# Performance work log

Measured on AMD Instinct MI355X. Metric: run time of the kernel, lower is better.

Reference implementation:

```python
import jax, jax.numpy as jnp
import numpy as np
import math

B, N, D_MODEL, H, D_HEAD = 2, 2048, 1024, 16, 64
EPS = 1e-6

def setup_inputs() -> dict:
    key = jax.random.key(0)
    ks = jax.random.split(key, 6)
    s = 1.0 / math.sqrt(D_MODEL)
    return {
        "X": jax.random.normal(ks[0], (B, N, D_MODEL), dtype=jnp.float32),
        "Wq": jax.random.normal(ks[1], (D_MODEL, H * D_HEAD), dtype=jnp.float32) * s,
        "Wk": jax.random.normal(ks[2], (D_MODEL, H * D_HEAD), dtype=jnp.float32) * s,
        "Wv": jax.random.normal(ks[3], (D_MODEL, H * D_HEAD), dtype=jnp.float32) * s,
        "Wo": jax.random.normal(ks[4], (H * D_HEAD, D_MODEL), dtype=jnp.float32) * s,
        "bo": jnp.zeros((D_MODEL,), dtype=jnp.float32),
    }

def reference(X, Wq, Wk, Wv, Wo, bo):
    b, n, _ = X.shape
    # project and split heads -> [b, h, n, d_head]
    def heads(Y):
        return Y.reshape(b, n, H, D_HEAD).transpose(0, 2, 1, 3)
    Q = heads(X @ Wq)
    K = heads(X @ Wk)
    V = heads(X @ Wv)
    # per-head L2 normalization of Q and K
    Q = Q / (jnp.linalg.norm(Q, axis=-1, keepdims=True) + EPS)
    K = K / (jnp.linalg.norm(K, axis=-1, keepdims=True) + EPS)
    # scores [b, h, n, n]
    A = jnp.einsum("bhqd,bhkd->bhqk", Q, K) / math.sqrt(D_HEAD)
    causal = jnp.triu(jnp.ones((n, n), dtype=bool), k=1)
    A = jnp.where(causal, -jnp.inf, A)
    A = jax.nn.softmax(A, axis=-1)
    V_hat = jnp.einsum("bhqk,bhkd->bhqd", A, V)
    V_hat = V_hat.transpose(0, 2, 1, 3).reshape(b, n, H * D_HEAD)
    return V_hat @ Wo + bo
```

## Files before the change

kernel.cpp:

```cpp
#include <hip/hip_runtime.h>
#include <hip/hip_bf16.h>
#include <math.h>

#define BATCH 2
#define NSEQ  2048
#define DM    1024
#define NH    16
#define DH    64
#define EPS_N 1e-6f

typedef unsigned short u16;
typedef __attribute__((ext_vector_type(8))) short short8;
typedef __attribute__((ext_vector_type(8))) unsigned short u16x8;
typedef __attribute__((ext_vector_type(4))) unsigned short u16x4;
typedef __attribute__((ext_vector_type(4))) float f32x4;

__device__ __forceinline__ u16 f2bf(float x) {
  __hip_bfloat16 h = __float2bfloat16(x);
  return *reinterpret_cast<u16*>(&h);
}

__device__ __forceinline__ void gl_lds16(const u16* g, u16* lds_base) {
  __builtin_amdgcn_global_load_lds(
      (__attribute__((address_space(1))) void*)g,
      (__attribute__((address_space(3))) void*)lds_base, 16, 0, 0);
}

__global__ __launch_bounds__(256) void prep(
    const float* __restrict__ X,
    const float* __restrict__ w0, const float* __restrict__ w1,
    const float* __restrict__ w2, const float* __restrict__ w3,
    u16* __restrict__ Xb, u16* __restrict__ WT) {
  const int id = blockIdx.x, tid = threadIdx.x;
  if (id >= 1024) {
    size_t base = ((size_t)(id - 1024) * 256 + tid) * 8;
    float4 f0 = *(const float4*)&X[base];
    float4 f1 = *(const float4*)&X[base + 4];
    u16x8 v;
    v[0] = f2bf(f0.x); v[1] = f2bf(f0.y); v[2] = f2bf(f0.z); v[3] = f2bf(f0.w);
    v[4] = f2bf(f1.x); v[5] = f2bf(f1.y); v[6] = f2bf(f1.z); v[7] = f2bf(f1.w);
    *(u16x8*)&Xb[base] = v;
    return;
  }
  const int z = id >> 8, xy = id & 255, bx = xy & 15, by = xy >> 4;
  const float* in = (z == 0) ? w0 : (z == 1) ? w1 : (z == 2) ? w2 : w3;
  u16* o = WT + (size_t)z * DM * DM;
  __shared__ u16 T[64][65];
  const int n0 = bx * 64, k0 = by * 64;
  #pragma unroll
  for (int i = 0; i < 4; i++) {
    int c = tid + 256 * i, row = c >> 4, col4 = c & 15;
    float4 f = *(const float4*)&in[(size_t)(k0 + row) * DM + n0 + col4 * 4];
    T[row][col4 * 4 + 0] = f2bf(f.x);
    T[row][col4 * 4 + 1] = f2bf(f.y);
    T[row][col4 * 4 + 2] = f2bf(f.z);
    T[row][col4 * 4 + 3] = f2bf(f.w);
  }
  __syncthreads();
  #pragma unroll
  for (int i = 0; i < 2; i++) {
    int c = tid + 256 * i, row = c >> 3, col8 = c & 7;
    u16x8 v;
    #pragma unroll
    for (int e = 0; e < 8; e++) v[e] = T[col8 * 8 + e][row];
    *(u16x8*)&o[(size_t)(n0 + row) * DM + k0 + col8 * 8] = v;
  }
}

#define GEMM128_MAINLOOP(Aptr, Btptr)                                          \
  __shared__ u16 As[128 * 64];                                                 \
  __shared__ u16 Bs[128 * 64];                                                 \
  const int tid = threadIdx.x, w = tid >> 6, lane = tid & 63;                  \
  const int ml = lane & 15, quad = lane >> 4;                                  \
  const int m0 = blockIdx.y * 128, n0 = blockIdx.x * 128;                      \
  const int wm = w & 1, wn = w >> 1;                                           \
  const int srow = lane >> 3;                      \
  const int scol = ((lane & 7) ^ srow) * 8;         \
  f32x4 acc[4][4];                                                             \
  _Pragma("unroll") for (int mi = 0; mi < 4; mi++)                             \
    _Pragma("unroll") for (int ni = 0; ni < 4; ni++)                           \
      _Pragma("unroll") for (int e = 0; e < 4; e++) acc[mi][ni][e] = 0.f;      \
  for (int k0 = 0; k0 < DM; k0 += 64) {                                        \
    __syncthreads();                                                           \
    _Pragma("unroll") for (int L = 0; L < 4; L++) {                            \
      int I = w * 4 + L;                                                       \
      gl_lds16(Aptr  + (size_t)(m0 + I * 8 + srow) * DM + k0 + scol,           \
               As + I * 512);                                                  \
      gl_lds16(Btptr + (size_t)(n0 + I * 8 + srow) * DM + k0 + scol,           \
               Bs + I * 512);                                                  \
    }                                                                          \
    __syncthreads();                                                           \
    _Pragma("unroll") for (int kk = 0; kk < 64; kk += 32) {                    \
      const int kc = kk >> 3;                          \
      short8 am[4], bn[4];                                                     \
      _Pragma("unroll") for (int i = 0; i < 4; i++) {                          \
        int ra = wm * 64 + i * 16 + ml;                                        \
        int rb = wn * 64 + i * 16 + ml;                                        \
        am[i] = *(const short8*)&As[ra * 64 + (((quad + kc) ^ (ra & 7)) * 8)]; \
        bn[i] = *(const short8*)&Bs[rb * 64 + (((quad + kc) ^ (rb & 7)) * 8)]; \
      }                                                                        \
      _Pragma("unroll") for (int mi = 0; mi < 4; mi++)                         \
        _Pragma("unroll") for (int ni = 0; ni < 4; ni++)                       \
          acc[mi][ni] = __builtin_amdgcn_mfma_f32_16x16x32_bf16(               \
              am[mi], bn[ni], acc[mi][ni], 0, 0, 0);                           \
    }                                                                          \
  }

__global__ __launch_bounds__(256) void gemm_qkv128(
    const u16* __restrict__ Xb, const u16* __restrict__ WT,
    u16* __restrict__ Qo, u16* __restrict__ Ko, u16* __restrict__ Vt) {
  const u16* Bt = WT + (size_t)blockIdx.z * DM * DM;
  GEMM128_MAINLOOP(Xb, Bt)
  const int z = blockIdx.z;
  if (z < 2) {
    u16* OutQK = (z == 0) ? Qo : Ko;
    const float qsc = (z == 0) ? 0.125f : 1.0f;
    const int h = (n0 >> 6) + wn;
    #pragma unroll
    for (int mi = 0; mi < 4; mi++) {
      int mrow0 = m0 + wm * 64 + mi * 16 + quad * 4;
      int b = mrow0 >> 11, tok0 = mrow0 & (NSEQ - 1);
      #pragma unroll
      for (int r = 0; r < 4; r++) {
        float ss = 0.f;
        #pragma unroll
        for (int ni = 0; ni < 4; ni++) ss += acc[mi][ni][r] * acc[mi][ni][r];
        ss += __shfl_xor(ss, 1, 64);
        ss += __shfl_xor(ss, 2, 64);
        ss += __shfl_xor(ss, 4, 64);
        ss += __shfl_xor(ss, 8, 64);
        float sc = qsc / (sqrtf(ss) + EPS_N);
        #pragma unroll
        for (int ni = 0; ni < 4; ni++)
          OutQK[((size_t)(b * NH + h) * NSEQ + tok0 + r) * DH + ni * 16 + ml] =
              f2bf(acc[mi][ni][r] * sc);
      }
    }
  } else {
    #pragma unroll
    for (int mi = 0; mi < 4; mi++) {
      int mrow0 = m0 + wm * 64 + mi * 16 + quad * 4;
      int b = mrow0 >> 11, tok0 = mrow0 & (NSEQ - 1);
      #pragma unroll
      for (int ni = 0; ni < 4; ni++) {
        int n = n0 + wn * 64 + ni * 16 + ml;
        int h = n >> 6, d = n & 63;
        u16x4 pk;
        #pragma unroll
        for (int r = 0; r < 4; r++) pk[r] = f2bf(acc[mi][ni][r]);
        *(u16x4*)&Vt[((size_t)(b * NH + h) * DH + d) * NSEQ + tok0] = pk;
      }
    }
  }
}

__global__ __launch_bounds__(256) void gemm_proj128(
    const u16* __restrict__ A, const u16* __restrict__ BtW,
    const float* __restrict__ bias, float* __restrict__ out) {
  GEMM128_MAINLOOP(A, BtW)
  #pragma unroll
  for (int ni = 0; ni < 4; ni++) {
    int n = n0 + wn * 64 + ni * 16 + ml;
    float bz = bias[n];
    #pragma unroll
    for (int mi = 0; mi < 4; mi++) {
      int mrow0 = m0 + wm * 64 + mi * 16 + quad * 4;
      #pragma unroll
      for (int r = 0; r < 4; r++)
        out[(size_t)(mrow0 + r) * DM + n] = acc[mi][ni][r] + bz;
    }
  }
}

__global__ __launch_bounds__(256) void flash_attn(
    const u16* __restrict__ Qb, const u16* __restrict__ Kb,
    const u16* __restrict__ Vt, u16* __restrict__ vhat) {
  const int tid = threadIdx.x, w = tid >> 6, lane = tid & 63;
  const int ml = lane & 15, quad = lane >> 4;
  const int wq = w & 1, wk = w >> 1;
  const int bh = blockIdx.x;
  const int bb = bh >> 4, hb = bh & 15;
  const int pair = blockIdx.y;
  const u16* Qh = Qb + (size_t)bh * NSEQ * DH;
  const u16* Kh = Kb + (size_t)bh * NSEQ * DH;
  const u16* Vth = Vt + (size_t)bh * DH * NSEQ;

  __shared__ u16 Ks [64][72];
  __shared__ u16 VsT[64][72];
  __shared__ u16 Ps [4][16][40];
  __shared__ float Os[2][16][66];
  __shared__ float Ls[2][16];

  const int vd = tid >> 2, vc = tid & 3;

  for (int ph = 0; ph < 2; ph++) {
    const int qb32 = ph ? (63 - pair) : pair;
    const int q0 = qb32 * 32;
    const int ntiles = (qb32 >> 1) + 1;

    short8 aq[2];
    #pragma unroll
    for (int c = 0; c < 2; c++)
      aq[c] = *(const short8*)&Qh[(size_t)(q0 + wq * 16 + ml) * DH + c * 32 + quad * 8];

    f32x4 oacc[4];
    #pragma unroll
    for (int n = 0; n < 4; n++)
      #pragma unroll
      for (int e = 0; e < 4; e++) oacc[n][e] = 0.f;
    float l_[4] = {0.f, 0.f, 0.f, 0.f};

    for (int t = 0; t < ntiles; t++) {
      const int j0 = t * 64;
      u16x8 kreg[2], vreg[2];
      #pragma unroll
      for (int i = 0; i < 2; i++) {
        kreg[i] = *(const u16x8*)&Kh[(size_t)(j0 + lane) * DH + (w + 4 * i) * 8];
        vreg[i] = *(const u16x8*)&Vth[(size_t)vd * NSEQ + j0 + (vc + 4 * i) * 8];
      }
      __syncthreads();
      #pragma unroll
      for (int i = 0; i < 2; i++) {
        *(u16x8*)&Ks[lane][(w + 4 * i) * 8] = kreg[i];
        *(u16x8*)&VsT[vd][(vc + 4 * i) * 8] = vreg[i];
      }
      __syncthreads();

      f32x4 sacc[2];
      #pragma unroll
      for (int n = 0; n < 2; n++)
        #pragma unroll
        for (int e = 0; e < 4; e++) sacc[n][e] = 0.f;
      #pragma unroll
      for (int c = 0; c < 2; c++)
        #pragma unroll
        for (int n = 0; n < 2; n++) {
          short8 bf = *(const short8*)&Ks[wk * 32 + n * 16 + ml][c * 32 + quad * 8];
          sacc[n] = __builtin_amdgcn_mfma_f32_16x16x32_bf16(aq[c], bf, sacc[n], 0, 0, 0);
        }

      const bool lastt = (t == ntiles - 1);
      float p[2][4];
      #pragma unroll
      for (int n = 0; n < 2; n++) {
        int j = j0 + wk * 32 + n * 16 + ml;
        #pragma unroll
        for (int r = 0; r < 4; r++) {
          int q = q0 + wq * 16 + quad * 4 + r;
          float e = __expf(sacc[n][r]);
          p[n][r] = (lastt && j > q) ? 0.f : e;
          l_[r] += p[n][r];
        }
      }

      #pragma unroll
      for (int n = 0; n < 2; n++)
        #pragma unroll
        for (int r = 0; r < 4; r++)
          Ps[w][quad * 4 + r][n * 16 + ml] = f2bf(p[n][r]);

      short8 ap = *(const short8*)&Ps[w][ml][quad * 8];
      #pragma unroll
      for (int n = 0; n < 4; n++) {
        short8 bv = *(const short8*)&VsT[n * 16 + ml][wk * 32 + quad * 8];
        oacc[n] = __builtin_amdgcn_mfma_f32_16x16x32_bf16(ap, bv, oacc[n], 0, 0, 0);
      }
    }

    float lred[4];
    #pragma unroll
    for (int r = 0; r < 4; r++) {
      float lv = l_[r];
      lv += __shfl_xor(lv, 1, 64);
      lv += __shfl_xor(lv, 2, 64);
      lv += __shfl_xor(lv, 4, 64);
      lv += __shfl_xor(lv, 8, 64);
      lred[r] = lv;
    }
    if (wk == 0) {
      #pragma unroll
      for (int n = 0; n < 4; n++)
        #pragma unroll
        for (int r = 0; r < 4; r++)
          Os[wq][quad * 4 + r][n * 16 + ml] = oacc[n][r];
      if (ml == 0) {
        #pragma unroll
        for (int r = 0; r < 4; r++) Ls[wq][quad * 4 + r] = lred[r];
      }
    }
    __syncthreads();
    if (wk == 1) {
      #pragma unroll
      for (int r = 0; r < 4; r++) {
        float inv = 1.f / (lred[r] + Ls[wq][quad * 4 + r]);
        int q = q0 + wq * 16 + quad * 4 + r;
        #pragma unroll
        for (int n = 0; n < 4; n++) {
          float o = oacc[n][r] + Os[wq][quad * 4 + r][n * 16 + ml];
          vhat[((size_t)(bb * NSEQ + q)) * DM + hb * DH + n * 16 + ml] =
              f2bf(o * inv);
        }
      }
    }
  }
}

extern "C" void kernel_launch(void* const* d_in, const int* in_sizes, int n_in,
                              void* d_out, int out_size, void* d_ws, size_t ws_size,
                              hipStream_t stream) {
  const float* X  = (const float*)d_in[0];
  const float* Wq = (const float*)d_in[1];
  const float* Wk = (const float*)d_in[2];
  const float* Wv = (const float*)d_in[3];
  const float* Wo = (const float*)d_in[4];
  const float* bo = (const float*)d_in[5];
  float* out = (float*)d_out;

  const size_t NE = (size_t)BATCH * NSEQ * DM;
  u16* Qb   = (u16*)d_ws;
  u16* Kb   = Qb + NE;
  u16* Vt   = Kb + NE;
  u16* XbVh = Vt + NE;
  u16* WT   = XbVh + NE;

  prep        <<<dim3(3072),      256, 0, stream>>>(X, Wq, Wk, Wv, Wo, XbVh, WT);
  gemm_qkv128 <<<dim3(8, 32, 3),  256, 0, stream>>>(XbVh, WT, Qb, Kb, Vt);
  flash_attn  <<<dim3(32, 32),    256, 0, stream>>>(Qb, Kb, Vt, XbVh);
  gemm_proj128<<<dim3(8, 32, 1),  256, 0, stream>>>(XbVh, WT + 3 * (size_t)DM * DM,
                                                    bo, out);
}
```

Before: 205.4 us.

## Load K/V MFMA fragments directly from global memory, drop LDS staging and barriers

```diff
diff --git a/kernel.cpp b/kernel.cpp
--- a/kernel.cpp
+++ b/kernel.cpp
@@ -172,7 +172,7 @@
   }
 }
 
-__global__ __launch_bounds__(256) void flash_attn(
+__global__ __launch_bounds__(256, 4) void flash_attn(
     const u16* __restrict__ Qb, const u16* __restrict__ Kb,
     const u16* __restrict__ Vt, u16* __restrict__ vhat) {
   const int tid = threadIdx.x, w = tid >> 6, lane = tid & 63;
@@ -185,13 +185,9 @@
   const u16* Kh = Kb + (size_t)bh * NSEQ * DH;
   const u16* Vth = Vt + (size_t)bh * DH * NSEQ;
 
-  __shared__ u16 Ks [64][72];
-  __shared__ u16 VsT[64][72];
   __shared__ u16 Ps [4][16][40];
   __shared__ float Os[2][16][66];
   __shared__ float Ls[2][16];
-
-  const int vd = tid >> 2, vc = tid & 3;
 
   for (int ph = 0; ph < 2; ph++) {
     const int qb32 = ph ? (63 - pair) : pair;
@@ -210,36 +206,48 @@
       for (int e = 0; e < 4; e++) oacc[n][e] = 0.f;
     float l_[4] = {0.f, 0.f, 0.f, 0.f};
 
+    const u16* kp  = Kh + (size_t)(wk * 32 + ml) * DH + quad * 8;
+    const u16* vp0 = Vth + (size_t)ml * NSEQ + wk * 32 + quad * 8;
+    const u16* vp1 = vp0 + (size_t)16 * NSEQ;
+    const u16* vp2 = vp0 + (size_t)32 * NSEQ;
+    const u16* vp3 = vp0 + (size_t)48 * NSEQ;
+
+    short8 kb[2][2];
+    #pragma unroll
+    for (int c = 0; c < 2; c++)
+      #pragma unroll
+      for (int n = 0; n < 2; n++)
+        kb[c][n] = *(const short8*)&kp[n * 16 * DH + c * 32];
+
     for (int t = 0; t < ntiles; t++) {
+      short8 vb[4];
+      vb[0] = *(const short8*)vp0; vp0 += 64;
+      vb[1] = *(const short8*)vp1; vp1 += 64;
+      vb[2] = *(const short8*)vp2; vp2 += 64;
+      vb[3] = *(const short8*)vp3; vp3 += 64;
+
+      f32x4 sacc[2];
+      #pragma unroll
+      for (int n = 0; n < 2; n++)
+        #pragma unroll
+        for (int e = 0; e < 4; e++) sacc[n][e] = 0.f;
+      #pragma unroll
+      for (int c = 0; c < 2; c++)
+        #pragma unroll
+        for (int n = 0; n < 2; n++)
+          sacc[n] = __builtin_amdgcn_mfma_f32_16x16x32_bf16(aq[c], kb[c][n], sacc[n], 0, 0, 0);
+
+      kp += 64 * DH;
+      if (t + 1 < ntiles) {
+        #pragma unroll
+        for (int c = 0; c < 2; c++)
+          #pragma unroll
+          for (int n = 0; n < 2; n++)
+            kb[c][n] = *(const short8*)&kp[n * 16 * DH + c * 32];
+      }
+
+      const bool lastt = (t == ntiles - 1);
       const int j0 = t * 64;
-      u16x8 kreg[2], vreg[2];
-      #pragma unroll
-      for (int i = 0; i < 2; i++) {
-        kreg[i] = *(const u16x8*)&Kh[(size_t)(j0 + lane) * DH + (w + 4 * i) * 8];
-        vreg[i] = *(const u16x8*)&Vth[(size_t)vd * NSEQ + j0 + (vc + 4 * i) * 8];
-      }
-      __syncthreads();
-      #pragma unroll
-      for (int i = 0; i < 2; i++) {
-        *(u16x8*)&Ks[lane][(w + 4 * i) * 8] = kreg[i];
-        *(u16x8*)&VsT[vd][(vc + 4 * i) * 8] = vreg[i];
-      }
-      __syncthreads();
-
-      f32x4 sacc[2];
-      #pragma unroll
-      for (int n = 0; n < 2; n++)
-        #pragma unroll
-        for (int e = 0; e < 4; e++) sacc[n][e] = 0.f;
-      #pragma unroll
-      for (int c = 0; c < 2; c++)
-        #pragma unroll
-        for (int n = 0; n < 2; n++) {
-          short8 bf = *(const short8*)&Ks[wk * 32 + n * 16 + ml][c * 32 + quad * 8];
-          sacc[n] = __builtin_amdgcn_mfma_f32_16x16x32_bf16(aq[c], bf, sacc[n], 0, 0, 0);
-        }
-
-      const bool lastt = (t == ntiles - 1);
       float p[2][4];
       #pragma unroll
       for (int n = 0; n < 2; n++) {
@@ -261,10 +269,8 @@
 
       short8 ap = *(const short8*)&Ps[w][ml][quad * 8];
       #pragma unroll
-      for (int n = 0; n < 4; n++) {
-        short8 bv = *(const short8*)&VsT[n * 16 + ml][wk * 32 + quad * 8];
-        oacc[n] = __builtin_amdgcn_mfma_f32_16x16x32_bf16(ap, bv, oacc[n], 0, 0, 0);
-      }
+      for (int n = 0; n < 4; n++)
+        oacc[n] = __builtin_amdgcn_mfma_f32_16x16x32_bf16(ap, vb[n], oacc[n], 0, 0, 0);
     }
 
     float lred[4];
@@ -302,6 +308,7 @@
         }
       }
     }
+    __syncthreads();
   }
 }
 
```

Measured after the change: 273.0 us. 32.9% more time.
